# Optimization experiments

Hardware: AMD Instinct MI355X
Metric: run time of the kernel (lower is better)

The kernel has to match this reference:

```python
import jax, jax.numpy as jnp
import numpy as np

HIDDEN = 1024
HEADS = 16
HEAD_DIM = HIDDEN // HEADS
B, S = 2, 1024


def setup_inputs() -> dict:
    key = jax.random.key(0)
    ks = jax.random.split(key, 14)
    sc = 1.0 / np.sqrt(HIDDEN)
    inp = {
        "q": jax.random.normal(ks[0], (B, S, HIDDEN), jnp.float32),
        "k": jax.random.normal(ks[1], (B, S, HIDDEN), jnp.float32),
        "v": jax.random.normal(ks[2], (B, S, HIDDEN), jnp.float32),
        "mask": jax.random.randint(ks[3], (B, S), 0, 2, jnp.int32),
        "shift": jax.random.normal(ks[4], (B * HEADS, S, S), jnp.float32) * 0.1,
        "wq": jax.random.normal(ks[5], (HIDDEN, HIDDEN), jnp.float32) * sc,
        "bq": jnp.zeros((HIDDEN,), jnp.float32),
        "wk": jax.random.normal(ks[6], (HIDDEN, HIDDEN), jnp.float32) * sc,
        "bk": jnp.zeros((HIDDEN,), jnp.float32),
        "wv": jax.random.normal(ks[7], (HIDDEN, HIDDEN), jnp.float32) * sc,
        "bv": jnp.zeros((HIDDEN,), jnp.float32),
        "wo": jax.random.normal(ks[8], (HIDDEN, HIDDEN), jnp.float32) * sc,
        "bo": jnp.zeros((HIDDEN,), jnp.float32),
    }
    return inp


def _to_heads(x):
    # (B,S,Dm) -> (B*H, S, Dh), batch-major over heads (b*H + h)
    b, s, _ = x.shape
    return x.reshape(b, s, HEADS, HEAD_DIM).transpose(0, 2, 1, 3).reshape(b * HEADS, s, HEAD_DIM)


def reference(q, k, v, mask, shift, wq, bq, wk, bk, wv, bv, wo, bo):
    b, s, dm = q.shape
    qh = _to_heads(q @ wq.T + bq)
    kh = _to_heads(k @ wk.T + bk)
    vh = _to_heads(v @ wv.T + bv)
    scores = jnp.einsum("bqd,bkd->bqk", qh, kh) / jnp.float32(np.sqrt(HEAD_DIM))
    scores = scores + shift
    # faithful to torch: mask tiled head-major (h*B + b) -> outer product m_i * m_j
    m = jnp.tile(mask, (HEADS, 1))  # (H*B, S)
    attn_mask = m[:, :, None] * m[:, None, :]  # (H*B, S, S)
    scores = jnp.where(attn_mask == 0, jnp.float32(-1e9), scores)
    p = jax.nn.softmax(scores, axis=-1)
    out = jnp.einsum("bqk,bkd->bqd", p, vh)
    out = out.reshape(b, HEADS, s, HEAD_DIM).transpose(0, 2, 1, 3).reshape(b, s, dm)
    return out @ wo.T + bo
```

## Files before the change

### kernel.cpp

```cpp
#include <hip/hip_runtime.h>
#include <hip/hip_bf16.h>

#define S_LEN 1024
#define DMODEL 1024
#define N_HEADS 16
#define D_HEAD 64
#define BATCH 2
#define N_BH 32

typedef __attribute__((ext_vector_type(8))) short short8;
typedef __attribute__((ext_vector_type(4))) float f32x4;
typedef __attribute__((ext_vector_type(4))) int i32x4;

static __device__ __forceinline__ unsigned short f2bf(float x) {
    unsigned int u = __float_as_uint(x);
    return (unsigned short)((u + 0x7fffu + ((u >> 16) & 1u)) >> 16);
}

static __device__ __forceinline__ float bf2f(unsigned short h) {
    return __uint_as_float(((unsigned int)h) << 16);
}

static __device__ __forceinline__ float sum8(short8 v) {
    float s = 0.f;
#pragma unroll
    for (int j = 0; j < 8; ++j) s += bf2f((unsigned short)v[j]);
    return s;
}

__global__ __launch_bounds__(256) void cvt_kernel(
    const float* __restrict__ wq, const float* __restrict__ wk,
    const float* __restrict__ wv, const float* __restrict__ wo,
    const float* __restrict__ q, const float* __restrict__ k,
    const float* __restrict__ v,
    unsigned short* __restrict__ Wb, unsigned short* __restrict__ Xb)
{
    const int z = blockIdx.y;
    const int idx = blockIdx.x * 256 + threadIdx.x;
    const float* src;
    unsigned short* dst;
    int n4;
    if (z < 4) {
        src = (z == 0) ? wq : (z == 1) ? wk : (z == 2) ? wv : wo;
        dst = Wb + (size_t)z * 1048576;
        n4 = 262144;
    } else {
        int j = z - 4;
        src = (j == 0) ? q : (j == 1) ? k : v;
        dst = Xb + (size_t)j * 2097152;
        n4 = 524288;
    }
    if (idx < n4) {
        f32x4 f = *reinterpret_cast<const f32x4*>(src + (size_t)idx * 4);
        ushort4 h = { f2bf(f[0]), f2bf(f[1]), f2bf(f[2]), f2bf(f[3]) };
        *reinterpret_cast<ushort4*>(dst + (size_t)idx * 4) = h;
    }
}

__device__ __forceinline__ void gemm_core(const unsigned short* __restrict__ A,
                                          const unsigned short* __restrict__ W,
                                          const float* __restrict__ bias,
                                          void* __restrict__ outp, int outmode,
                                          int n0, int j0)
{
    __shared__ unsigned short As[128 * 40];
    __shared__ unsigned short Bs[128 * 40];
    const int t = threadIdx.x;
    const int lane = t & 63, w = t >> 6;
    const int wm = w >> 1, wn = w & 1;
    const int g = lane >> 4, r = lane & 15;
    const int srow = t >> 2, seg = t & 3;

    f32x4 acc[4][4];
#pragma unroll
    for (int mi = 0; mi < 4; ++mi)
#pragma unroll
        for (int ni = 0; ni < 4; ++ni)
            acc[mi][ni] = (f32x4){0.f, 0.f, 0.f, 0.f};

    for (int ks = 0; ks < DMODEL / 32; ++ks) {
        const int k0 = ks * 32;
        __syncthreads();
#pragma unroll
        for (int i = 0; i < 2; ++i) {
            *reinterpret_cast<short8*>(&As[(srow + i * 64) * 40 + seg * 8]) =
                *reinterpret_cast<const short8*>(A + (size_t)(n0 + srow + i * 64) * DMODEL + k0 + seg * 8);
            *reinterpret_cast<short8*>(&Bs[(srow + i * 64) * 40 + seg * 8]) =
                *reinterpret_cast<const short8*>(W + (size_t)(j0 + srow + i * 64) * DMODEL + k0 + seg * 8);
        }
        __syncthreads();
        short8 af[4], bf[4];
#pragma unroll
        for (int mi = 0; mi < 4; ++mi)
            af[mi] = *reinterpret_cast<const short8*>(&As[(wm * 64 + mi * 16 + r) * 40 + g * 8]);
#pragma unroll
        for (int ni = 0; ni < 4; ++ni)
            bf[ni] = *reinterpret_cast<const short8*>(&Bs[(wn * 64 + ni * 16 + r) * 40 + g * 8]);
#pragma unroll
        for (int mi = 0; mi < 4; ++mi)
#pragma unroll
            for (int ni = 0; ni < 4; ++ni)
                acc[mi][ni] = __builtin_amdgcn_mfma_f32_16x16x32_bf16(af[mi], bf[ni], acc[mi][ni], 0, 0, 0);
    }

#pragma unroll
    for (int mi = 0; mi < 4; ++mi) {
#pragma unroll
        for (int ni = 0; ni < 4; ++ni) {
            int col = j0 + wn * 64 + ni * 16 + r;
            float bv = bias[col];
#pragma unroll
            for (int t4 = 0; t4 < 4; ++t4) {
                int n = n0 + wm * 64 + mi * 16 + g * 4 + t4;
                float v = acc[mi][ni][t4] + bv;
                if (outmode == 2) {
                    ((float*)outp)[(size_t)n * DMODEL + col] = v;
                } else {
                    int b_ = n >> 10, s_ = n & 1023;
                    int h_ = col >> 6, dh = col & 63;
                    if (outmode == 0)
                        ((unsigned short*)outp)[((size_t)(b_ * N_HEADS + h_) * S_LEN + s_) * D_HEAD + dh] = f2bf(v);
                    else
                        ((unsigned short*)outp)[((size_t)(b_ * N_HEADS + h_) * D_HEAD + dh) * S_LEN + s_] = f2bf(v);
                }
            }
        }
    }
}

__global__ __launch_bounds__(256) void qkv_kernel(
    const unsigned short* __restrict__ Xb, const unsigned short* __restrict__ Wb,
    const float* __restrict__ bq, const float* __restrict__ bk, const float* __restrict__ bv,
    unsigned short* Qh, unsigned short* Kh, unsigned short* Vt)
{
    const int z = blockIdx.z;
    const unsigned short* A = Xb + (size_t)z * 2097152;
    const unsigned short* W = Wb + (size_t)z * 1048576;
    const float* bias = (z == 0) ? bq : (z == 1) ? bk : bv;
    void* outp = (z == 0) ? (void*)Qh : (z == 1) ? (void*)Kh : (void*)Vt;
    gemm_core(A, W, bias, outp, (z == 2) ? 1 : 0, blockIdx.x * 128, blockIdx.y * 128);
}

__global__ __launch_bounds__(256) void oproj_kernel(
    const unsigned short* __restrict__ attn, const unsigned short* __restrict__ Wo,
    const float* __restrict__ bo, float* out)
{
    gemm_core(attn, Wo, bo, (void*)out, 2, blockIdx.x * 128, blockIdx.y * 128);
}

__global__ __launch_bounds__(256) void score_kernel(
    const unsigned short* __restrict__ Qh, const unsigned short* __restrict__ Kh,
    const int* __restrict__ mask, const float* __restrict__ shift,
    unsigned short* __restrict__ Sbuf, int bh0)
{
    __shared__ union {
        struct { unsigned short As[128 * 72]; unsigned short Bs[64 * 72]; } st;
        float C[128 * 68];
    } u;
    const int zloc = blockIdx.z;
    const int bh = bh0 + zloc;
    const int q0 = blockIdx.x * 128, j0 = blockIdx.y * 64;
    const int t = threadIdx.x, lane = t & 63, w = t >> 6;
    const int wm = w >> 1, wn = w & 1, g = lane >> 4, r = lane & 15;
    const unsigned short* Qb = Qh + (size_t)bh * S_LEN * D_HEAD;
    const unsigned short* Kb = Kh + (size_t)bh * S_LEN * D_HEAD;
    unsigned short* Sl = Sbuf + (size_t)zloc * S_LEN * S_LEN;
    const int* mrow = mask + (bh & (BATCH - 1)) * S_LEN;

    {
        int row = t >> 3, seg = t & 7;
#pragma unroll
        for (int i = 0; i < 4; ++i)
            *reinterpret_cast<short8*>(&u.st.As[(row + i * 32) * 72 + seg * 8]) =
                *reinterpret_cast<const short8*>(Qb + (size_t)(q0 + row + i * 32) * D_HEAD + seg * 8);
#pragma unroll
        for (int i = 0; i < 2; ++i)
            *reinterpret_cast<short8*>(&u.st.Bs[(row + i * 32) * 72 + seg * 8]) =
                *reinterpret_cast<const short8*>(Kb + (size_t)(j0 + row + i * 32) * D_HEAD + seg * 8);
    }
    __syncthreads();

    f32x4 acc[4][2];
#pragma unroll
    for (int mi = 0; mi < 4; ++mi)
#pragma unroll
        for (int ni = 0; ni < 2; ++ni)
            acc[mi][ni] = (f32x4){0.f, 0.f, 0.f, 0.f};

#pragma unroll
    for (int ks = 0; ks < 2; ++ks) {
        short8 af[4], bf[2];
#pragma unroll
        for (int mi = 0; mi < 4; ++mi)
            af[mi] = *reinterpret_cast<const short8*>(&u.st.As[(wm * 64 + mi * 16 + r) * 72 + ks * 32 + g * 8]);
#pragma unroll
        for (int ni = 0; ni < 2; ++ni)
            bf[ni] = *reinterpret_cast<const short8*>(&u.st.Bs[(wn * 32 + ni * 16 + r) * 72 + ks * 32 + g * 8]);
#pragma unroll
        for (int mi = 0; mi < 4; ++mi)
#pragma unroll
            for (int ni = 0; ni < 2; ++ni)
                acc[mi][ni] = __builtin_amdgcn_mfma_f32_16x16x32_bf16(af[mi], bf[ni], acc[mi][ni], 0, 0, 0);
    }
    __syncthreads();

#pragma unroll
    for (int mi = 0; mi < 4; ++mi)
#pragma unroll
        for (int ni = 0; ni < 2; ++ni)
#pragma unroll
            for (int t4 = 0; t4 < 4; ++t4)
                u.C[(wm * 64 + mi * 16 + g * 4 + t4) * 68 + wn * 32 + ni * 16 + r] = acc[mi][ni][t4];
    __syncthreads();

#pragma unroll
    for (int c = 0; c < 8; ++c) {
        int flat = c * 1024 + t * 4;
        int row = flat >> 6;
        int col = flat & 63;
        f32x4 cv = *reinterpret_cast<const f32x4*>(&u.C[row * 68 + col]);
        f32x4 sv = *reinterpret_cast<const f32x4*>(
            shift + ((size_t)bh * S_LEN + q0 + row) * S_LEN + j0 + col);
        i32x4 mk = *reinterpret_cast<const i32x4*>(mrow + j0 + col);
        int mq = mrow[q0 + row];
        float p0 = (mq & mk[0]) ? __expf(fmaf(cv[0], 0.125f, sv[0])) : 0.f;
        float p1 = (mq & mk[1]) ? __expf(fmaf(cv[1], 0.125f, sv[1])) : 0.f;
        float p2 = (mq & mk[2]) ? __expf(fmaf(cv[2], 0.125f, sv[2])) : 0.f;
        float p3 = (mq & mk[3]) ? __expf(fmaf(cv[3], 0.125f, sv[3])) : 0.f;
        if (mq == 0) { p0 = p1 = p2 = p3 = 1.f; }
        ushort4 pk = { f2bf(p0), f2bf(p1), f2bf(p2), f2bf(p3) };
        *reinterpret_cast<ushort4*>(Sl + (size_t)(q0 + row) * S_LEN + j0 + col) = pk;
    }
}

__global__ __launch_bounds__(256) void pv_kernel(
    const unsigned short* __restrict__ Sbuf, const unsigned short* __restrict__ Vt,
    unsigned short* __restrict__ attnbuf, int bh0)
{
    __shared__ unsigned short Ss[2][64 * 72];
    __shared__ unsigned short Vs[2][64 * 72];
    __shared__ float Lsum[64];
    const int zloc = blockIdx.y;
    const int bh = bh0 + zloc;
    const int q0 = blockIdx.x * 64;
    const int b_ = bh >> 4, h_ = bh & 15;
    const int t = threadIdx.x, lane = t & 63, w = t >> 6;
    const int wm = w >> 1, wn = w & 1, g = lane >> 4, r = lane & 15;
    const unsigned short* Sl = Sbuf + (size_t)zloc * S_LEN * S_LEN;
    const unsigned short* Vb = Vt + (size_t)bh * D_HEAD * S_LEN;
    const int srow = t >> 3, seg = t & 7;

    float rs0 = 0.f, rs1 = 0.f;
    f32x4 acc[2][2];
#pragma unroll
    for (int mi = 0; mi < 2; ++mi)
#pragma unroll
        for (int ni = 0; ni < 2; ++ni)
            acc[mi][ni] = (f32x4){0.f, 0.f, 0.f, 0.f};

    {
        short8 sv0 = *reinterpret_cast<const short8*>(Sl + (size_t)(q0 + srow) * S_LEN + seg * 8);
        short8 sv1 = *reinterpret_cast<const short8*>(Sl + (size_t)(q0 + srow + 32) * S_LEN + seg * 8);
        short8 vv0 = *reinterpret_cast<const short8*>(Vb + (size_t)srow * S_LEN + seg * 8);
        short8 vv1 = *reinterpret_cast<const short8*>(Vb + (size_t)(srow + 32) * S_LEN + seg * 8);
        *reinterpret_cast<short8*>(&Ss[0][srow * 72 + seg * 8]) = sv0;
        *reinterpret_cast<short8*>(&Ss[0][(srow + 32) * 72 + seg * 8]) = sv1;
        *reinterpret_cast<short8*>(&Vs[0][srow * 72 + seg * 8]) = vv0;
        *reinterpret_cast<short8*>(&Vs[0][(srow + 32) * 72 + seg * 8]) = vv1;
        rs0 += sum8(sv0);
        rs1 += sum8(sv1);
    }
    __syncthreads();

    for (int kt = 0; kt < 16; ++kt) {
        const int cur = kt & 1;
        short8 sv0, sv1, vv0, vv1;
        if (kt < 15) {
            const int k0 = (kt + 1) * 64;
            sv0 = *reinterpret_cast<const short8*>(Sl + (size_t)(q0 + srow) * S_LEN + k0 + seg * 8);
            sv1 = *reinterpret_cast<const short8*>(Sl + (size_t)(q0 + srow + 32) * S_LEN + k0 + seg * 8);
            vv0 = *reinterpret_cast<const short8*>(Vb + (size_t)srow * S_LEN + k0 + seg * 8);
            vv1 = *reinterpret_cast<const short8*>(Vb + (size_t)(srow + 32) * S_LEN + k0 + seg * 8);
        }
#pragma unroll
        for (int ks = 0; ks < 2; ++ks) {
            short8 af[2], bf[2];
#pragma unroll
            for (int mi = 0; mi < 2; ++mi)
                af[mi] = *reinterpret_cast<const short8*>(&Ss[cur][(wm * 32 + mi * 16 + r) * 72 + ks * 32 + g * 8]);
#pragma unroll
            for (int ni = 0; ni < 2; ++ni)
                bf[ni] = *reinterpret_cast<const short8*>(&Vs[cur][(wn * 32 + ni * 16 + r) * 72 + ks * 32 + g * 8]);
#pragma unroll
            for (int mi = 0; mi < 2; ++mi)
#pragma unroll
                for (int ni = 0; ni < 2; ++ni)
                    acc[mi][ni] = __builtin_amdgcn_mfma_f32_16x16x32_bf16(af[mi], bf[ni], acc[mi][ni], 0, 0, 0);
        }
        if (kt < 15) {
            *reinterpret_cast<short8*>(&Ss[cur ^ 1][srow * 72 + seg * 8]) = sv0;
            *reinterpret_cast<short8*>(&Ss[cur ^ 1][(srow + 32) * 72 + seg * 8]) = sv1;
            *reinterpret_cast<short8*>(&Vs[cur ^ 1][srow * 72 + seg * 8]) = vv0;
            *reinterpret_cast<short8*>(&Vs[cur ^ 1][(srow + 32) * 72 + seg * 8]) = vv1;
            rs0 += sum8(sv0);
            rs1 += sum8(sv1);
        }
        __syncthreads();
    }

    rs0 += __shfl_xor(rs0, 1); rs0 += __shfl_xor(rs0, 2); rs0 += __shfl_xor(rs0, 4);
    rs1 += __shfl_xor(rs1, 1); rs1 += __shfl_xor(rs1, 2); rs1 += __shfl_xor(rs1, 4);
    if (seg == 0) { Lsum[srow] = rs0; Lsum[srow + 32] = rs1; }
    __syncthreads();

#pragma unroll
    for (int mi = 0; mi < 2; ++mi)
#pragma unroll
        for (int ni = 0; ni < 2; ++ni)
#pragma unroll
            for (int t4 = 0; t4 < 4; ++t4) {
                int row = wm * 32 + mi * 16 + g * 4 + t4;
                int col = wn * 32 + ni * 16 + r;
                float o = acc[mi][ni][t4] / Lsum[row];
                attnbuf[((size_t)(b_ * S_LEN + q0 + row)) * DMODEL + h_ * D_HEAD + col] = f2bf(o);
            }
}

extern "C" void kernel_launch(void* const* d_in, const int* in_sizes, int n_in,
                              void* d_out, int out_size, void* d_ws, size_t ws_size,
                              hipStream_t stream)
{
    const float* q     = (const float*)d_in[0];
    const float* k     = (const float*)d_in[1];
    const float* v     = (const float*)d_in[2];
    const int*   mask  = (const int*)d_in[3];
    const float* shift = (const float*)d_in[4];
    const float* wq    = (const float*)d_in[5];
    const float* bq    = (const float*)d_in[6];
    const float* wk    = (const float*)d_in[7];
    const float* bk    = (const float*)d_in[8];
    const float* wv    = (const float*)d_in[9];
    const float* bv    = (const float*)d_in[10];
    const float* wo    = (const float*)d_in[11];
    const float* bo    = (const float*)d_in[12];
    float* out = (float*)d_out;

    const size_t nhalf = (size_t)N_BH * S_LEN * D_HEAD;
    unsigned short* Qh = (unsigned short*)d_ws;
    unsigned short* Kh = Qh + nhalf;
    unsigned short* Vt = Kh + nhalf;
    unsigned short* attnbuf = Vt + nhalf;
    unsigned short* Wb = attnbuf + (size_t)BATCH * S_LEN * DMODEL;
    unsigned short* Xb = Wb + (size_t)4 * 1048576;
    unsigned short* Sbuf = Xb + (size_t)3 * 2097152;

    const size_t base = 36u * 1024 * 1024;
    const size_t sbytes = (size_t)S_LEN * S_LEN * 2;
    int CH = 1;
    if (ws_size > base) {
        size_t c = (ws_size - base) / sbytes;
        CH = (c >= 32) ? 32 : (c < 1 ? 1 : (int)c);
    }

    dim3 blk(256);
    cvt_kernel<<<dim3(2048, 7), blk, 0, stream>>>(wq, wk, wv, wo, q, k, v, Wb, Xb);
    qkv_kernel<<<dim3(16, 8, 3), blk, 0, stream>>>(Xb, Wb, bq, bk, bv, Qh, Kh, Vt);
    for (int bh0 = 0; bh0 < N_BH; bh0 += CH) {
        int c = (N_BH - bh0 < CH) ? (N_BH - bh0) : CH;
        score_kernel<<<dim3(8, 16, c), blk, 0, stream>>>(Qh, Kh, mask, shift, Sbuf, bh0);
        pv_kernel<<<dim3(16, c), blk, 0, stream>>>(Sbuf, Vt, attnbuf, bh0);
    }
    oproj_kernel<<<dim3(16, 8), blk, 0, stream>>>(attnbuf, Wb + (size_t)3 * 1048576, bo, out);
}
```

Baseline: 139.9 us.

## Restructure score kernel to full-row 16-query tiles with staged shift and XCD-aware block mapping

Each score block now handles 16 query rows across all 1024 keys. Q fragments are held in registers and the 64KB shift slab is staged into LDS with an XOR swizzle, while K fragments are read directly from global memory. MFMA results are packed to bf16 through a small per-wave LDS buffer so the probability stores to global are coalesced 16-byte writes. Both the score and PV kernels remap block indices when the full 32-head grid is used, so neighbouring heads and queries land on the same XCD for L2 locality. The trade is large per-block LDS use, which lowers occupancy, and K rows being re-read from global by every block.

```diff
diff --git a/kernel.cpp b/kernel.cpp
--- a/kernel.cpp
+++ b/kernel.cpp
@@ -153,83 +153,65 @@
     const int* __restrict__ mask, const float* __restrict__ shift,
     unsigned short* __restrict__ Sbuf, int bh0)
 {
-    __shared__ union {
-        struct { unsigned short As[128 * 72]; unsigned short Bs[64 * 72]; } st;
-        float C[128 * 68];
-    } u;
-    const int zloc = blockIdx.z;
+    __shared__ __align__(16) float Shs[16 * 1024];
+    __shared__ unsigned short Plds[4][16][72];
+    int fb = blockIdx.y * 64 + blockIdx.x;
+    int zloc, qg;
+    if (gridDim.y == 32) {
+        int l = (fb & 7) * 256 + (fb >> 3);
+        zloc = l >> 6; qg = l & 63;
+    } else { zloc = blockIdx.y; qg = blockIdx.x; }
     const int bh = bh0 + zloc;
-    const int q0 = blockIdx.x * 128, j0 = blockIdx.y * 64;
+    const int q0 = qg * 16;
     const int t = threadIdx.x, lane = t & 63, w = t >> 6;
-    const int wm = w >> 1, wn = w & 1, g = lane >> 4, r = lane & 15;
+    const int g = lane >> 4, r = lane & 15;
+
     const unsigned short* Qb = Qh + (size_t)bh * S_LEN * D_HEAD;
     const unsigned short* Kb = Kh + (size_t)bh * S_LEN * D_HEAD;
     unsigned short* Sl = Sbuf + (size_t)zloc * S_LEN * S_LEN;
-    const int* mrow = mask + (bh & (BATCH - 1)) * S_LEN;
-
-    {
-        int row = t >> 3, seg = t & 7;
-#pragma unroll
-        for (int i = 0; i < 4; ++i)
-            *reinterpret_cast<short8*>(&u.st.As[(row + i * 32) * 72 + seg * 8]) =
-                *reinterpret_cast<const short8*>(Qb + (size_t)(q0 + row + i * 32) * D_HEAD + seg * 8);
-#pragma unroll
-        for (int i = 0; i < 2; ++i)
-            *reinterpret_cast<short8*>(&u.st.Bs[(row + i * 32) * 72 + seg * 8]) =
-                *reinterpret_cast<const short8*>(Kb + (size_t)(j0 + row + i * 32) * D_HEAD + seg * 8);
+    const float* shb = shift + (size_t)bh * S_LEN * S_LEN;
+    const int* mp = mask + (bh & (BATCH - 1)) * S_LEN;
+
+    short8 qf0 = *reinterpret_cast<const short8*>(&Qb[(size_t)(q0 + r) * D_HEAD + g * 8]);
+    short8 qf1 = *reinterpret_cast<const short8*>(&Qb[(size_t)(q0 + r) * D_HEAD + 32 + g * 8]);
+    const int mq = mp[q0 + r];
+
+#pragma unroll 4
+    for (int j = 0; j < 16; ++j) {
+        f32x4 v = *reinterpret_cast<const f32x4*>(shb + (size_t)(q0 + j) * S_LEN + t * 4);
+        *reinterpret_cast<f32x4*>(&Shs[j * 1024 + (t ^ j) * 4]) = v;
     }
     __syncthreads();
 
-    f32x4 acc[4][2];
-#pragma unroll
-    for (int mi = 0; mi < 4; ++mi)
-#pragma unroll
-        for (int ni = 0; ni < 2; ++ni)
-            acc[mi][ni] = (f32x4){0.f, 0.f, 0.f, 0.f};
-
-#pragma unroll
-    for (int ks = 0; ks < 2; ++ks) {
-        short8 af[4], bf[2];
-#pragma unroll
-        for (int mi = 0; mi < 4; ++mi)
-            af[mi] = *reinterpret_cast<const short8*>(&u.st.As[(wm * 64 + mi * 16 + r) * 72 + ks * 32 + g * 8]);
-#pragma unroll
-        for (int ni = 0; ni < 2; ++ni)
-            bf[ni] = *reinterpret_cast<const short8*>(&u.st.Bs[(wn * 32 + ni * 16 + r) * 72 + ks * 32 + g * 8]);
-#pragma unroll
-        for (int mi = 0; mi < 4; ++mi)
-#pragma unroll
-            for (int ni = 0; ni < 2; ++ni)
-                acc[mi][ni] = __builtin_amdgcn_mfma_f32_16x16x32_bf16(af[mi], bf[ni], acc[mi][ni], 0, 0, 0);
-    }
-    __syncthreads();
-
-#pragma unroll
-    for (int mi = 0; mi < 4; ++mi)
-#pragma unroll
-        for (int ni = 0; ni < 2; ++ni)
-#pragma unroll
-            for (int t4 = 0; t4 < 4; ++t4)
-                u.C[(wm * 64 + mi * 16 + g * 4 + t4) * 68 + wn * 32 + ni * 16 + r] = acc[mi][ni][t4];
-    __syncthreads();
-
-#pragma unroll
-    for (int c = 0; c < 8; ++c) {
-        int flat = c * 1024 + t * 4;
-        int row = flat >> 6;
-        int col = flat & 63;
-        f32x4 cv = *reinterpret_cast<const f32x4*>(&u.C[row * 68 + col]);
-        f32x4 sv = *reinterpret_cast<const f32x4*>(
-            shift + ((size_t)bh * S_LEN + q0 + row) * S_LEN + j0 + col);
-        i32x4 mk = *reinterpret_cast<const i32x4*>(mrow + j0 + col);
-        int mq = mrow[q0 + row];
-        float p0 = (mq & mk[0]) ? __expf(fmaf(cv[0], 0.125f, sv[0])) : 0.f;
-        float p1 = (mq & mk[1]) ? __expf(fmaf(cv[1], 0.125f, sv[1])) : 0.f;
-        float p2 = (mq & mk[2]) ? __expf(fmaf(cv[2], 0.125f, sv[2])) : 0.f;
-        float p3 = (mq & mk[3]) ? __expf(fmaf(cv[3], 0.125f, sv[3])) : 0.f;
-        if (mq == 0) { p0 = p1 = p2 = p3 = 1.f; }
-        ushort4 pk = { f2bf(p0), f2bf(p1), f2bf(p2), f2bf(p3) };
-        *reinterpret_cast<ushort4*>(Sl + (size_t)(q0 + row) * S_LEN + j0 + col) = pk;
+    for (int cc = 0; cc < 4; ++cc) {
+        const int kbase = w * 256 + cc * 64;
+#pragma unroll
+        for (int fn = 0; fn < 4; ++fn) {
+            short8 kv0 = *reinterpret_cast<const short8*>(&Kb[(size_t)(kbase + fn * 16 + r) * D_HEAD + g * 8]);
+            short8 kv1 = *reinterpret_cast<const short8*>(&Kb[(size_t)(kbase + fn * 16 + r) * D_HEAD + 32 + g * 8]);
+            f32x4 a = (f32x4){0.f, 0.f, 0.f, 0.f};
+            a = __builtin_amdgcn_mfma_f32_16x16x32_bf16(kv0, qf0, a, 0, 0, 0);
+            a = __builtin_amdgcn_mfma_f32_16x16x32_bf16(kv1, qf1, a, 0, 0, 0);
+            int gran = (kbase >> 2) + fn * 4 + g;
+            f32x4 shv = *reinterpret_cast<const f32x4*>(&Shs[r * 1024 + (gran ^ r) * 4]);
+            i32x4 mk = *reinterpret_cast<const i32x4*>(mp + kbase + fn * 16 + g * 4);
+            float p0 = (mq & mk[0]) ? __expf(fmaf(a[0], 0.125f, shv[0])) : 0.f;
+            float p1 = (mq & mk[1]) ? __expf(fmaf(a[1], 0.125f, shv[1])) : 0.f;
+            float p2 = (mq & mk[2]) ? __expf(fmaf(a[2], 0.125f, shv[2])) : 0.f;
+            float p3 = (mq & mk[3]) ? __expf(fmaf(a[3], 0.125f, shv[3])) : 0.f;
+            if (mq == 0) { p0 = p1 = p2 = p3 = 1.f; }
+            ushort4 pk = { f2bf(p0), f2bf(p1), f2bf(p2), f2bf(p3) };
+            *reinterpret_cast<ushort4*>(&Plds[w][r][fn * 16 + g * 4]) = pk;
+        }
+        asm volatile("s_waitcnt lgkmcnt(0)" ::: "memory");
+        __builtin_amdgcn_sched_barrier(0);
+        {
+            int row = lane & 15, qq = lane >> 4;
+            short8 s0 = *reinterpret_cast<const short8*>(&Plds[w][row][qq * 16]);
+            short8 s1 = *reinterpret_cast<const short8*>(&Plds[w][row][qq * 16 + 8]);
+            *reinterpret_cast<short8*>(Sl + (size_t)(q0 + row) * S_LEN + kbase + qq * 16) = s0;
+            *reinterpret_cast<short8*>(Sl + (size_t)(q0 + row) * S_LEN + kbase + qq * 16 + 8) = s1;
+        }
     }
 }
 
@@ -240,9 +222,14 @@
     __shared__ unsigned short Ss[2][64 * 72];
     __shared__ unsigned short Vs[2][64 * 72];
     __shared__ float Lsum[64];
-    const int zloc = blockIdx.y;
+    int fb = blockIdx.y * 16 + blockIdx.x;
+    int zloc, qxb;
+    if (gridDim.y == 32) {
+        int l = (fb & 7) * 64 + (fb >> 3);
+        zloc = l >> 4; qxb = l & 15;
+    } else { zloc = blockIdx.y; qxb = blockIdx.x; }
     const int bh = bh0 + zloc;
-    const int q0 = blockIdx.x * 64;
+    const int q0 = qxb * 64;
     const int b_ = bh >> 4, h_ = bh & 15;
     const int t = threadIdx.x, lane = t & 63, w = t >> 6;
     const int wm = w >> 1, wn = w & 1, g = lane >> 4, r = lane & 15;
@@ -367,7 +354,7 @@
     qkv_kernel<<<dim3(16, 8, 3), blk, 0, stream>>>(Xb, Wb, bq, bk, bv, Qh, Kh, Vt);
     for (int bh0 = 0; bh0 < N_BH; bh0 += CH) {
         int c = (N_BH - bh0 < CH) ? (N_BH - bh0) : CH;
-        score_kernel<<<dim3(8, 16, c), blk, 0, stream>>>(Qh, Kh, mask, shift, Sbuf, bh0);
+        score_kernel<<<dim3(64, c), blk, 0, stream>>>(Qh, Kh, mask, shift, Sbuf, bh0);
         pv_kernel<<<dim3(16, c), blk, 0, stream>>>(Sbuf, Vt, attnbuf, bh0);
     }
     oproj_kernel<<<dim3(16, 8), blk, 0, stream>>>(attnbuf, Wb + (size_t)3 * 1048576, bo, out);
```

Result: slower. 157.3 us (+12.4%).
